# Performance work log

Measured on AMD Instinct MI355X. Metric: run time of the kernel, lower is better.

Reference implementation:

```python
import jax, jax.numpy as jnp
import numpy as np

NUM_TAGS = 5
START_TAG = 3  # ent_to_ix['<START>']
STOP_TAG = 4   # ent_to_ix['<STOP>']
NEG_INF = -10000.0
B, T = 8192, 512


def setup_inputs() -> dict:
    key = jax.random.key(0)
    k1, k2 = jax.random.split(key)
    feats = jax.random.normal(k1, (B, T, NUM_TAGS), dtype=jnp.float32)
    transitions = jax.random.normal(k2, (NUM_TAGS, NUM_TAGS), dtype=jnp.float32)
    # matches __init__: no transition into START, none out of STOP
    transitions = transitions.at[START_TAG, :].set(NEG_INF)
    transitions = transitions.at[:, STOP_TAG].set(NEG_INF)
    return {"feats": feats, "transitions": transitions}


def reference(feats, transitions):
    """Batched CRF forward algorithm (log partition function).

    feats: [B, T, K] emission scores; transitions: [K, K] where
    transitions[next, prev] is the score of prev -> next.
    Returns alpha: [B] log partition per sequence.
    """
    def single(seq):  # seq: [T, K]
        init = jnp.full((NUM_TAGS,), NEG_INF, dtype=seq.dtype).at[START_TAG].set(0.0)

        def step(forward_var, feat):
            # scores[next, prev] = forward_var[prev] + transitions[next, prev] + feat[next]
            scores = forward_var[None, :] + transitions + feat[:, None]
            return jax.nn.logsumexp(scores, axis=1), None

        forward_var, _ = jax.lax.scan(step, init, seq)
        terminal = forward_var + transitions[STOP_TAG]
        return jax.nn.logsumexp(terminal)

    return jax.vmap(single)(feats)
```

## Files before the change

### kernel.cpp

```cpp
#include <hip/hip_runtime.h>

#define BB 8192
#define SEQF 2560

__device__ __forceinline__ float rfl(float x) {
    return __int_as_float(__builtin_amdgcn_readfirstlane(__float_as_int(x)));
}

__global__ __launch_bounds__(256, 4) void crf_fused(const float* __restrict__ feats,
                                                    const float* __restrict__ trans,
                                                    float* __restrict__ out) {
    const int tid  = threadIdx.x;
    const int lane = tid & 63;
    const int half = lane >> 5;
    const int cpos = lane & 31;
    const int gw   = blockIdx.x * 4 + (tid >> 6);
    const int s0   = gw * 2;

    const float4* p = (const float4*)(feats + (size_t)(s0 + half) * SEQF) + cpos * 20;
    float4 q0 =p[0],  q1 =p[1],  q2 =p[2],  q3 =p[3],  q4 =p[4];
    float4 q5 =p[5],  q6 =p[6],  q7 =p[7],  q8 =p[8],  q9 =p[9];
    float4 q10=p[10], q11=p[11], q12=p[12], q13=p[13], q14=p[14];
    float4 q15=p[15], q16=p[16], q17=p[17], q18=p[18], q19=p[19];
    __builtin_amdgcn_sched_barrier(0);

    const float E00=rfl(__expf(trans[0])),  E01=rfl(__expf(trans[1])),  E02=rfl(__expf(trans[2]));
    const float E10=rfl(__expf(trans[5])),  E11=rfl(__expf(trans[6])),  E12=rfl(__expf(trans[7]));
    const float E20=rfl(__expf(trans[10])), E21=rfl(__expf(trans[11])), E22=rfl(__expf(trans[12]));
    const float C0 =rfl(__expf(trans[3])),  C1 =rfl(__expf(trans[8])),  C2 =rfl(__expf(trans[13]));
    const float S0 =rfl(__expf(trans[20])), S1 =rfl(__expf(trans[21])), S2 =rfl(__expf(trans[22]));

    const bool c0 = (cpos == 0);
    const float G00 = c0 ? C0 : E00, G01 = c0 ? C0 : E01, G02 = c0 ? C0 : E02;
    const float G10 = c0 ? C1 : E10, G11 = c0 ? C1 : E11, G12 = c0 ? C1 : E12;
    const float G20 = c0 ? C2 : E20, G21 = c0 ? C2 : E21, G22 = c0 ? C2 : E22;

#define CRF_STEP(FA, FB, FC) do {                                   \
        float e0 = __expf(FA), e1 = __expf(FB), e2 = __expf(FC);    \
        float N00 = e0 * (E00*M00 + E01*M10 + E02*M20);             \
        float N01 = e0 * (E00*M01 + E01*M11 + E02*M21);             \
        float N02 = e0 * (E00*M02 + E01*M12 + E02*M22);             \
        float N10 = e1 * (E10*M00 + E11*M10 + E12*M20);             \
        float N11 = e1 * (E10*M01 + E11*M11 + E12*M21);             \
        float N12 = e1 * (E10*M02 + E11*M12 + E12*M22);             \
        float N20 = e2 * (E20*M00 + E21*M10 + E22*M20);             \
        float N21 = e2 * (E20*M01 + E21*M11 + E22*M21);             \
        float N22 = e2 * (E20*M02 + E21*M12 + E22*M22);             \
        M00=N00; M01=N01; M02=N02;                                  \
        M10=N10; M11=N11; M12=N12;                                  \
        M20=N20; M21=N21; M22=N22;                                  \
    } while (0)

#define CRF_RENORM() do {                                           \
        float mx = fmaxf(fmaxf(fmaxf(M00,M01), fmaxf(M02,M10)),     \
                         fmaxf(fmaxf(M11,M12), fmaxf(fmaxf(M20,M21),M22))); \
        mx = fmaxf(mx, 1e-30f);                                     \
        int ee = (int)((__float_as_uint(mx) >> 23) & 0xffu) - 127;  \
        float sc = __uint_as_float((unsigned)(127 - ee) << 23);     \
        ls += (float)ee;                                            \
        M00*=sc; M01*=sc; M02*=sc;                                  \
        M10*=sc; M11*=sc; M12*=sc;                                  \
        M20*=sc; M21*=sc; M22*=sc;                                  \
    } while (0)

#define TREE_LEVEL(D, RN) do {                                      \
        float P00=__shfl_down(M00,D), P01=__shfl_down(M01,D), P02=__shfl_down(M02,D); \
        float P10=__shfl_down(M10,D), P11=__shfl_down(M11,D), P12=__shfl_down(M12,D); \
        float P20=__shfl_down(M20,D), P21=__shfl_down(M21,D), P22=__shfl_down(M22,D); \
        float Pls=__shfl_down(ls, D);                               \
        float N00 = P00*M00 + P01*M10 + P02*M20;                    \
        float N01 = P00*M01 + P01*M11 + P02*M21;                    \
        float N02 = P00*M02 + P01*M12 + P02*M22;                    \
        float N10 = P10*M00 + P11*M10 + P12*M20;                    \
        float N11 = P10*M01 + P11*M11 + P12*M21;                    \
        float N12 = P10*M02 + P11*M12 + P12*M22;                    \
        float N20 = P20*M00 + P21*M10 + P22*M20;                    \
        float N21 = P20*M01 + P21*M11 + P22*M21;                    \
        float N22 = P20*M02 + P21*M12 + P22*M22;                    \
        M00=N00; M01=N01; M02=N02; M10=N10; M11=N11; M12=N12;       \
        M20=N20; M21=N21; M22=N22;                                  \
        ls += Pls;                                                  \
        if (RN) CRF_RENORM();                                       \
    } while (0)

    float M00, M01, M02, M10, M11, M12, M20, M21, M22;
    float ls = 0.0f;

    {
        float e0 = __expf(q0.x), e1 = __expf(q0.y), e2 = __expf(q0.z);
        M00 = e0*G00; M01 = e0*G01; M02 = e0*G02;
        M10 = e1*G10; M11 = e1*G11; M12 = e1*G12;
        M20 = e2*G20; M21 = e2*G21; M22 = e2*G22;
    }
    CRF_STEP(q1.y,  q1.z,  q1.w);
    CRF_STEP(q2.z,  q2.w,  q3.x);
    CRF_STEP(q3.w,  q4.x,  q4.y);
    CRF_STEP(q5.x,  q5.y,  q5.z);
    CRF_STEP(q6.y,  q6.z,  q6.w);
    CRF_STEP(q7.z,  q7.w,  q8.x);
    CRF_STEP(q8.w,  q9.x,  q9.y);
    CRF_RENORM();
    CRF_STEP(q10.x, q10.y, q10.z);
    CRF_STEP(q11.y, q11.z, q11.w);
    CRF_STEP(q12.z, q12.w, q13.x);
    CRF_STEP(q13.w, q14.x, q14.y);
    CRF_STEP(q15.x, q15.y, q15.z);
    CRF_STEP(q16.y, q16.z, q16.w);
    CRF_STEP(q17.z, q17.w, q18.x);
    CRF_STEP(q18.w, q19.x, q19.y);
    CRF_RENORM();

    TREE_LEVEL(1, 0);
    TREE_LEVEL(2, 1);
    TREE_LEVEL(4, 0);
    TREE_LEVEL(8, 1);
    TREE_LEVEL(16, 1);

    float r = S0*M00 + S1*M10 + S2*M20;
    float res = __logf(r) + ls * 0.69314718055994531f;
    if (cpos == 0) out[s0 + half] = res;

#undef CRF_STEP
#undef CRF_RENORM
#undef TREE_LEVEL
}

extern "C" void kernel_launch(void* const* d_in, const int* in_sizes, int n_in,
                              void* d_out, int out_size, void* d_ws, size_t ws_size,
                              hipStream_t stream) {
    const float* feats = (const float*)d_in[0];
    const float* trans = (const float*)d_in[1];
    float* out = (float*)d_out;
    (void)d_ws; (void)ws_size;

    crf_fused<<<BB / 8, 256, 0, stream>>>(feats, trans, out);
}
```

Measured before the change: 19.60 us.

## Coalesce feature loads and transpose chunks through swizzled LDS per wave

Each wave now loads its two sequences with fully coalesced float4 reads (lane-contiguous), then writes them into a per-wave LDS buffer with an XOR swizzle and reads them back so each lane gets its contiguous 20-float4 chunk. Sequences are interleaved across lanes (lane parity selects sequence), so the tree reduction shifts to strides 2..32. Block size drops to 128 threads with more blocks, and LDS use grows to about 40KB per block. This trades strided 320-byte-per-lane global reads for extra LDS traffic and may reduce occupancy.

```diff
diff --git a/kernel.cpp b/kernel.cpp
--- a/kernel.cpp
+++ b/kernel.cpp
@@ -1,27 +1,30 @@
 #include <hip/hip_runtime.h>
 
 #define BB 8192
+#define TT 512
 #define SEQF 2560
+#define WLDS 1280
 
 __device__ __forceinline__ float rfl(float x) {
     return __int_as_float(__builtin_amdgcn_readfirstlane(__float_as_int(x)));
 }
 
-__global__ __launch_bounds__(256, 4) void crf_fused(const float* __restrict__ feats,
+__global__ __launch_bounds__(128, 4) void crf_fused(const float* __restrict__ feats,
                                                     const float* __restrict__ trans,
                                                     float* __restrict__ out) {
+    __shared__ __align__(16) float4 sm[2 * WLDS];
+
     const int tid  = threadIdx.x;
     const int lane = tid & 63;
-    const int half = lane >> 5;
-    const int cpos = lane & 31;
-    const int gw   = blockIdx.x * 4 + (tid >> 6);
-    const int s0   = gw * 2;
+    const int wv   = tid >> 6;
+    const int s0   = (blockIdx.x * 2 + wv) * 2;
 
-    const float4* p = (const float4*)(feats + (size_t)(s0 + half) * SEQF) + cpos * 20;
-    float4 q0 =p[0],  q1 =p[1],  q2 =p[2],  q3 =p[3],  q4 =p[4];
-    float4 q5 =p[5],  q6 =p[6],  q7 =p[7],  q8 =p[8],  q9 =p[9];
-    float4 q10=p[10], q11=p[11], q12=p[12], q13=p[13], q14=p[14];
-    float4 q15=p[15], q16=p[16], q17=p[17], q18=p[18], q19=p[19];
+    float4* wb = &sm[wv * WLDS];
+
+    const float4* gp = (const float4*)(feats + (size_t)s0 * SEQF);
+    float4 h[20];
+    #pragma unroll
+    for (int k = 0; k < 20; ++k) h[k] = gp[k * 64 + lane];
     __builtin_amdgcn_sched_barrier(0);
 
     const float E00=rfl(__expf(trans[0])),  E01=rfl(__expf(trans[1])),  E02=rfl(__expf(trans[2]));
@@ -30,7 +33,24 @@
     const float C0 =rfl(__expf(trans[3])),  C1 =rfl(__expf(trans[8])),  C2 =rfl(__expf(trans[13]));
     const float S0 =rfl(__expf(trans[20])), S1 =rfl(__expf(trans[21])), S2 =rfl(__expf(trans[22]));
 
-    const bool c0 = (cpos == 0);
+    #pragma unroll
+    for (int k = 0; k < 20; ++k) {
+        int G = k * 64 + lane;
+        int s = G >> 9;
+        s = G / 640;
+        int g = G - s * 640;
+        int c = g / 20;
+        int j = g - c * 20;
+        wb[j * 64 + (((c << 1) + s) ^ (j & 7))] = h[k];
+    }
+    __builtin_amdgcn_sched_barrier(0);
+
+    float4 q[20];
+    #pragma unroll
+    for (int j = 0; j < 20; ++j)
+        q[j] = wb[j * 64 + (lane ^ (j & 7))];
+
+    const bool c0 = (lane >> 1) == 0;
     const float G00 = c0 ? C0 : E00, G01 = c0 ? C0 : E01, G02 = c0 ? C0 : E02;
     const float G10 = c0 ? C1 : E10, G11 = c0 ? C1 : E11, G12 = c0 ? C1 : E12;
     const float G20 = c0 ? C2 : E20, G21 = c0 ? C2 : E21, G22 = c0 ? C2 : E22;
@@ -87,38 +107,38 @@
     float ls = 0.0f;
 
     {
-        float e0 = __expf(q0.x), e1 = __expf(q0.y), e2 = __expf(q0.z);
+        float e0 = __expf(q[0].x), e1 = __expf(q[0].y), e2 = __expf(q[0].z);
         M00 = e0*G00; M01 = e0*G01; M02 = e0*G02;
         M10 = e1*G10; M11 = e1*G11; M12 = e1*G12;
         M20 = e2*G20; M21 = e2*G21; M22 = e2*G22;
     }
-    CRF_STEP(q1.y,  q1.z,  q1.w);
-    CRF_STEP(q2.z,  q2.w,  q3.x);
-    CRF_STEP(q3.w,  q4.x,  q4.y);
-    CRF_STEP(q5.x,  q5.y,  q5.z);
-    CRF_STEP(q6.y,  q6.z,  q6.w);
-    CRF_STEP(q7.z,  q7.w,  q8.x);
-    CRF_STEP(q8.w,  q9.x,  q9.y);
+    CRF_STEP(q[1].y,  q[1].z,  q[1].w);
+    CRF_STEP(q[2].z,  q[2].w,  q[3].x);
+    CRF_STEP(q[3].w,  q[4].x,  q[4].y);
+    CRF_STEP(q[5].x,  q[5].y,  q[5].z);
+    CRF_STEP(q[6].y,  q[6].z,  q[6].w);
+    CRF_STEP(q[7].z,  q[7].w,  q[8].x);
+    CRF_STEP(q[8].w,  q[9].x,  q[9].y);
     CRF_RENORM();
-    CRF_STEP(q10.x, q10.y, q10.z);
-    CRF_STEP(q11.y, q11.z, q11.w);
-    CRF_STEP(q12.z, q12.w, q13.x);
-    CRF_STEP(q13.w, q14.x, q14.y);
-    CRF_STEP(q15.x, q15.y, q15.z);
-    CRF_STEP(q16.y, q16.z, q16.w);
-    CRF_STEP(q17.z, q17.w, q18.x);
-    CRF_STEP(q18.w, q19.x, q19.y);
+    CRF_STEP(q[10].x, q[10].y, q[10].z);
+    CRF_STEP(q[11].y, q[11].z, q[11].w);
+    CRF_STEP(q[12].z, q[12].w, q[13].x);
+    CRF_STEP(q[13].w, q[14].x, q[14].y);
+    CRF_STEP(q[15].x, q[15].y, q[15].z);
+    CRF_STEP(q[16].y, q[16].z, q[16].w);
+    CRF_STEP(q[17].z, q[17].w, q[18].x);
+    CRF_STEP(q[18].w, q[19].x, q[19].y);
     CRF_RENORM();
 
-    TREE_LEVEL(1, 0);
-    TREE_LEVEL(2, 1);
-    TREE_LEVEL(4, 0);
-    TREE_LEVEL(8, 1);
+    TREE_LEVEL(2, 0);
+    TREE_LEVEL(4, 1);
+    TREE_LEVEL(8, 0);
     TREE_LEVEL(16, 1);
+    TREE_LEVEL(32, 1);
 
     float r = S0*M00 + S1*M10 + S2*M20;
     float res = __logf(r) + ls * 0.69314718055994531f;
-    if (cpos == 0) out[s0 + half] = res;
+    if ((lane >> 1) == 0) out[s0 + (lane & 1)] = res;
 
 #undef CRF_STEP
 #undef CRF_RENORM
@@ -133,5 +153,5 @@
     float* out = (float*)d_out;
     (void)d_ws; (void)ws_size;
 
-    crf_fused<<<BB / 8, 256, 0, stream>>>(feats, trans, out);
+    crf_fused<<<BB / 4, 128, 0, stream>>>(feats, trans, out);
 }
```

Result: slower. 22.20 us (+13.3%).

## Pack CRF transfer-matrix math into float2 vectors with bias scaling and fewer renorms

Applied to the files above, without the earlier changes.

Groups two columns of the 3x3 transfer matrix into float2 vectors so the compiler can emit packed FP32 operations on the step and tree-combine math. Every transition exponent is scaled by e^-2, and 1024 (512 steps times 2) is added back to the result, which keeps values centred and allows one mid-sequence and some tree-level renormalisations to be dropped. The block size is halved to 128 threads with twice as many blocks. The risks are overflow or underflow if the bias does not match the input statistics, and the packed code may not map well to the hardware.

```diff
diff --git a/kernel.cpp b/kernel.cpp
--- a/kernel.cpp
+++ b/kernel.cpp
@@ -3,19 +3,22 @@
 #define BB 8192
 #define SEQF 2560
 
+typedef float v2f __attribute__((ext_vector_type(2)));
+
 __device__ __forceinline__ float rfl(float x) {
     return __int_as_float(__builtin_amdgcn_readfirstlane(__float_as_int(x)));
 }
+__device__ __forceinline__ v2f vsplat(float x) { return (v2f){x, x}; }
 
-__global__ __launch_bounds__(256, 4) void crf_fused(const float* __restrict__ feats,
+__global__ __launch_bounds__(128, 4) void crf_fused(const float* __restrict__ feats,
                                                     const float* __restrict__ trans,
                                                     float* __restrict__ out) {
     const int tid  = threadIdx.x;
     const int lane = tid & 63;
     const int half = lane >> 5;
     const int cpos = lane & 31;
-    const int gw   = blockIdx.x * 4 + (tid >> 6);
-    const int s0   = gw * 2;
+    const int wv   = tid >> 6;
+    const int s0   = (blockIdx.x * 2 + wv) * 2;
 
     const float4* p = (const float4*)(feats + (size_t)(s0 + half) * SEQF) + cpos * 20;
     float4 q0 =p[0],  q1 =p[1],  q2 =p[2],  q3 =p[3],  q4 =p[4];
@@ -24,73 +27,74 @@
     float4 q15=p[15], q16=p[16], q17=p[17], q18=p[18], q19=p[19];
     __builtin_amdgcn_sched_barrier(0);
 
-    const float E00=rfl(__expf(trans[0])),  E01=rfl(__expf(trans[1])),  E02=rfl(__expf(trans[2]));
-    const float E10=rfl(__expf(trans[5])),  E11=rfl(__expf(trans[6])),  E12=rfl(__expf(trans[7]));
-    const float E20=rfl(__expf(trans[10])), E21=rfl(__expf(trans[11])), E22=rfl(__expf(trans[12]));
-    const float C0 =rfl(__expf(trans[3])),  C1 =rfl(__expf(trans[8])),  C2 =rfl(__expf(trans[13]));
+    const float BIAS = 0.13533528323661270f;
+    const float E00=rfl(__expf(trans[0])*BIAS),  E01=rfl(__expf(trans[1])*BIAS),  E02=rfl(__expf(trans[2])*BIAS);
+    const float E10=rfl(__expf(trans[5])*BIAS),  E11=rfl(__expf(trans[6])*BIAS),  E12=rfl(__expf(trans[7])*BIAS);
+    const float E20=rfl(__expf(trans[10])*BIAS), E21=rfl(__expf(trans[11])*BIAS), E22=rfl(__expf(trans[12])*BIAS);
+    const float C0 =rfl(__expf(trans[3])*BIAS),  C1 =rfl(__expf(trans[8])*BIAS),  C2 =rfl(__expf(trans[13])*BIAS);
     const float S0 =rfl(__expf(trans[20])), S1 =rfl(__expf(trans[21])), S2 =rfl(__expf(trans[22]));
 
+    const v2f E00p=vsplat(E00), E01p=vsplat(E01), E02p=vsplat(E02);
+    const v2f E10p=vsplat(E10), E11p=vsplat(E11), E12p=vsplat(E12);
+    const v2f E20p=vsplat(E20), E21p=vsplat(E21), E22p=vsplat(E22);
+
     const bool c0 = (cpos == 0);
-    const float G00 = c0 ? C0 : E00, G01 = c0 ? C0 : E01, G02 = c0 ? C0 : E02;
-    const float G10 = c0 ? C1 : E10, G11 = c0 ? C1 : E11, G12 = c0 ? C1 : E12;
-    const float G20 = c0 ? C2 : E20, G21 = c0 ? C2 : E21, G22 = c0 ? C2 : E22;
+    const v2f GA0 = c0 ? vsplat(C0) : (v2f){E00, E01};
+    const v2f GA1 = c0 ? vsplat(C1) : (v2f){E10, E11};
+    const v2f GA2 = c0 ? vsplat(C2) : (v2f){E20, E21};
+    const float GB0 = c0 ? C0 : E02;
+    const float GB1 = c0 ? C1 : E12;
+    const float GB2 = c0 ? C2 : E22;
+
+    v2f MA0, MA1, MA2;
+    float MB0, MB1, MB2;
+    float ls = 0.0f;
 
 #define CRF_STEP(FA, FB, FC) do {                                   \
         float e0 = __expf(FA), e1 = __expf(FB), e2 = __expf(FC);    \
-        float N00 = e0 * (E00*M00 + E01*M10 + E02*M20);             \
-        float N01 = e0 * (E00*M01 + E01*M11 + E02*M21);             \
-        float N02 = e0 * (E00*M02 + E01*M12 + E02*M22);             \
-        float N10 = e1 * (E10*M00 + E11*M10 + E12*M20);             \
-        float N11 = e1 * (E10*M01 + E11*M11 + E12*M21);             \
-        float N12 = e1 * (E10*M02 + E11*M12 + E12*M22);             \
-        float N20 = e2 * (E20*M00 + E21*M10 + E22*M20);             \
-        float N21 = e2 * (E20*M01 + E21*M11 + E22*M21);             \
-        float N22 = e2 * (E20*M02 + E21*M12 + E22*M22);             \
-        M00=N00; M01=N01; M02=N02;                                  \
-        M10=N10; M11=N11; M12=N12;                                  \
-        M20=N20; M21=N21; M22=N22;                                  \
+        v2f NA0 = vsplat(e0) * (E00p*MA0 + E01p*MA1 + E02p*MA2);    \
+        v2f NA1 = vsplat(e1) * (E10p*MA0 + E11p*MA1 + E12p*MA2);    \
+        v2f NA2 = vsplat(e2) * (E20p*MA0 + E21p*MA1 + E22p*MA2);    \
+        float NB0 = e0 * (E00*MB0 + E01*MB1 + E02*MB2);             \
+        float NB1 = e1 * (E10*MB0 + E11*MB1 + E12*MB2);             \
+        float NB2 = e2 * (E20*MB0 + E21*MB1 + E22*MB2);             \
+        MA0=NA0; MA1=NA1; MA2=NA2; MB0=NB0; MB1=NB1; MB2=NB2;       \
     } while (0)
 
 #define CRF_RENORM() do {                                           \
-        float mx = fmaxf(fmaxf(fmaxf(M00,M01), fmaxf(M02,M10)),     \
-                         fmaxf(fmaxf(M11,M12), fmaxf(fmaxf(M20,M21),M22))); \
-        mx = fmaxf(mx, 1e-30f);                                     \
-        int ee = (int)((__float_as_uint(mx) >> 23) & 0xffu) - 127;  \
+        v2f mp = __builtin_elementwise_max(__builtin_elementwise_max(MA0, MA1), MA2); \
+        float mm = fmaxf(fmaxf(mp.x, mp.y), fmaxf(fmaxf(MB0, MB1), MB2)); \
+        mm = fmaxf(mm, 1e-30f);                                     \
+        int ee = (int)((__float_as_uint(mm) >> 23) & 0xffu) - 127;  \
         float sc = __uint_as_float((unsigned)(127 - ee) << 23);     \
         ls += (float)ee;                                            \
-        M00*=sc; M01*=sc; M02*=sc;                                  \
-        M10*=sc; M11*=sc; M12*=sc;                                  \
-        M20*=sc; M21*=sc; M22*=sc;                                  \
+        v2f scp = vsplat(sc);                                       \
+        MA0*=scp; MA1*=scp; MA2*=scp; MB0*=sc; MB1*=sc; MB2*=sc;    \
     } while (0)
 
 #define TREE_LEVEL(D, RN) do {                                      \
-        float P00=__shfl_down(M00,D), P01=__shfl_down(M01,D), P02=__shfl_down(M02,D); \
-        float P10=__shfl_down(M10,D), P11=__shfl_down(M11,D), P12=__shfl_down(M12,D); \
-        float P20=__shfl_down(M20,D), P21=__shfl_down(M21,D), P22=__shfl_down(M22,D); \
+        v2f PA0, PA1, PA2;                                          \
+        PA0.x=__shfl_down(MA0.x,D); PA0.y=__shfl_down(MA0.y,D);     \
+        PA1.x=__shfl_down(MA1.x,D); PA1.y=__shfl_down(MA1.y,D);     \
+        PA2.x=__shfl_down(MA2.x,D); PA2.y=__shfl_down(MA2.y,D);     \
+        float PB0=__shfl_down(MB0,D), PB1=__shfl_down(MB1,D), PB2=__shfl_down(MB2,D); \
         float Pls=__shfl_down(ls, D);                               \
-        float N00 = P00*M00 + P01*M10 + P02*M20;                    \
-        float N01 = P00*M01 + P01*M11 + P02*M21;                    \
-        float N02 = P00*M02 + P01*M12 + P02*M22;                    \
-        float N10 = P10*M00 + P11*M10 + P12*M20;                    \
-        float N11 = P10*M01 + P11*M11 + P12*M21;                    \
-        float N12 = P10*M02 + P11*M12 + P12*M22;                    \
-        float N20 = P20*M00 + P21*M10 + P22*M20;                    \
-        float N21 = P20*M01 + P21*M11 + P22*M21;                    \
-        float N22 = P20*M02 + P21*M12 + P22*M22;                    \
-        M00=N00; M01=N01; M02=N02; M10=N10; M11=N11; M12=N12;       \
-        M20=N20; M21=N21; M22=N22;                                  \
+        v2f NA0 = vsplat(PA0.x)*MA0 + vsplat(PA0.y)*MA1 + vsplat(PB0)*MA2; \
+        v2f NA1 = vsplat(PA1.x)*MA0 + vsplat(PA1.y)*MA1 + vsplat(PB1)*MA2; \
+        v2f NA2 = vsplat(PA2.x)*MA0 + vsplat(PA2.y)*MA1 + vsplat(PB2)*MA2; \
+        float NB0 = PA0.x*MB0 + PA0.y*MB1 + PB0*MB2;                \
+        float NB1 = PA1.x*MB0 + PA1.y*MB1 + PB1*MB2;                \
+        float NB2 = PA2.x*MB0 + PA2.y*MB1 + PB2*MB2;                \
+        MA0=NA0; MA1=NA1; MA2=NA2; MB0=NB0; MB1=NB1; MB2=NB2;       \
         ls += Pls;                                                  \
         if (RN) CRF_RENORM();                                       \
     } while (0)
 
-    float M00, M01, M02, M10, M11, M12, M20, M21, M22;
-    float ls = 0.0f;
-
     {
         float e0 = __expf(q0.x), e1 = __expf(q0.y), e2 = __expf(q0.z);
-        M00 = e0*G00; M01 = e0*G01; M02 = e0*G02;
-        M10 = e1*G10; M11 = e1*G11; M12 = e1*G12;
-        M20 = e2*G20; M21 = e2*G21; M22 = e2*G22;
+        MA0 = vsplat(e0) * GA0;  MB0 = e0 * GB0;
+        MA1 = vsplat(e1) * GA1;  MB1 = e1 * GB1;
+        MA2 = vsplat(e2) * GA2;  MB2 = e2 * GB2;
     }
     CRF_STEP(q1.y,  q1.z,  q1.w);
     CRF_STEP(q2.z,  q2.w,  q3.x);
@@ -99,7 +103,6 @@
     CRF_STEP(q6.y,  q6.z,  q6.w);
     CRF_STEP(q7.z,  q7.w,  q8.x);
     CRF_STEP(q8.w,  q9.x,  q9.y);
-    CRF_RENORM();
     CRF_STEP(q10.x, q10.y, q10.z);
     CRF_STEP(q11.y, q11.z, q11.w);
     CRF_STEP(q12.z, q12.w, q13.x);
@@ -111,13 +114,13 @@
     CRF_RENORM();
 
     TREE_LEVEL(1, 0);
-    TREE_LEVEL(2, 1);
-    TREE_LEVEL(4, 0);
-    TREE_LEVEL(8, 1);
+    TREE_LEVEL(2, 0);
+    TREE_LEVEL(4, 1);
+    TREE_LEVEL(8, 0);
     TREE_LEVEL(16, 1);
 
-    float r = S0*M00 + S1*M10 + S2*M20;
-    float res = __logf(r) + ls * 0.69314718055994531f;
+    float r = S0*MA0.x + S1*MA1.x + S2*MA2.x;
+    float res = __logf(r) + ls * 0.69314718055994531f + 1024.0f;
     if (cpos == 0) out[s0 + half] = res;
 
 #undef CRF_STEP
@@ -133,5 +136,5 @@
     float* out = (float*)d_out;
     (void)d_ws; (void)ws_size;
 
-    crf_fused<<<BB / 8, 256, 0, stream>>>(feats, trans, out);
+    crf_fused<<<BB / 4, 128, 0, stream>>>(feats, trans, out);
 }
```

Result: no change. 19.59 us (-0.0%).
